# Performance work log

Hardware: AMD Instinct MI355X
Metric: run time of the kernel (lower is better)

The kernel has to match this reference:

```python
import jax, jax.numpy as jnp
import numpy as np

N = 100000   # nodes
E = 1600000  # edges
IN = 128     # input_dim
H = 64       # hidden_dim
C = 10       # num_classes
L = 4        # num_layers
G = 200      # graphs in batch
BN_EPS = 1e-5


def setup_inputs() -> dict:
    key = jax.random.key(0)
    ks = jax.random.split(key, 12)
    s = 0.05
    h = jax.random.normal(ks[0], (N, IN), jnp.float32)
    snorm_n = jax.random.uniform(ks[1], (N, 1), jnp.float32)
    src = jax.random.randint(ks[2], (E,), 0, N, jnp.int32)
    dst = jax.random.randint(ks[3], (E,), 0, N, jnp.int32)
    graph_ids = jnp.sort(jax.random.randint(ks[4], (N,), 0, G, jnp.int32))
    W_embed = jax.random.normal(ks[5], (IN, H), jnp.float32) * s
    b_embed = jnp.zeros((H,), jnp.float32)
    eps = jnp.zeros((L,), jnp.float32)               # learnable eps, init 0
    W1 = jax.random.normal(ks[6], (L, H, H), jnp.float32) * s
    b1 = jnp.zeros((L, H), jnp.float32)
    g1 = jnp.ones((L, H), jnp.float32)               # MLP-internal BN gamma
    be1 = jnp.zeros((L, H), jnp.float32)             # MLP-internal BN beta
    W2 = jax.random.normal(ks[7], (L, H, H), jnp.float32) * s
    b2 = jnp.zeros((L, H), jnp.float32)
    g2 = jnp.ones((L, H), jnp.float32)               # bn_node_h gamma
    be2 = jnp.zeros((L, H), jnp.float32)             # bn_node_h beta
    Wlin = jax.random.normal(ks[8], (L + 1, H, C), jnp.float32) * s
    blin = jnp.zeros((L + 1, C), jnp.float32)
    return dict(h=h, snorm_n=snorm_n, src=src, dst=dst, graph_ids=graph_ids,
                W_embed=W_embed, b_embed=b_embed, eps=eps,
                W1=W1, b1=b1, g1=g1, be1=be1, W2=W2, b2=b2, g2=g2, be2=be2,
                Wlin=Wlin, blin=blin)


def _batchnorm(x, gamma, beta):
    # training-mode BatchNorm1d over the node axis
    m = jnp.mean(x, axis=0)
    v = jnp.mean(jnp.square(x - m), axis=0)
    return gamma * (x - m) * jax.lax.rsqrt(v + BN_EPS) + beta


def reference(h, snorm_n, src, dst, graph_ids, W_embed, b_embed, eps,
              W1, b1, g1, be1, W2, b2, g2, be2, Wlin, blin):
    # node embedding
    h = h @ W_embed + b_embed                                   # [N, H]
    hidden_rep = [h]
    for i in range(L):
        h_in = h
        # copy_u + sum reduce: neigh[v] = sum_{(u->v)} h[u]
        neigh = jax.ops.segment_sum(h[src], dst, num_segments=N)  # [N, H]
        h = (1.0 + eps[i]) * h + neigh
        # apply_func: 2-layer MLP with internal BN+ReLU (standard GIN MLP)
        h = jax.nn.relu(_batchnorm(h @ W1[i] + b1[i], g1[i], be1[i]))
        h = h @ W2[i] + b2[i]
        h = h * snorm_n                                          # graph_norm
        h = _batchnorm(h, g2[i], be2[i])                         # bn_node_h
        h = jax.nn.relu(h)
        h = h_in + h                                             # residual
        # dropout p=0.0 -> identity
        hidden_rep.append(h)
    score = jnp.zeros((G, C), h.dtype)
    for i, hr in enumerate(hidden_rep):
        pooled = jax.ops.segment_sum(hr, graph_ids, num_segments=G)  # SumPooling
        score = score + pooled @ Wlin[i] + blin[i]
    return score
```

## Files before the change

### kernel.cpp

```cpp
#include <hip/hip_runtime.h>
#include <hip/hip_bf16.h>
#include <math.h>

#define NN 100000
#define NE 1600000
#define KIN 128
#define HD 64
#define NC 10
#define NL 4
#define NG 200
#define NBKT 196

typedef short s16x8 __attribute__((ext_vector_type(8)));
typedef float f32x4 __attribute__((ext_vector_type(4)));
using f4 = float4;

static __device__ __forceinline__ ushort f2bf(float x) {
  __hip_bfloat16 b = __float2bfloat16(x);
  return *reinterpret_cast<ushort*>(&b);
}
static __device__ __forceinline__ float bf2f(ushort u) {
  return __uint_as_float(((unsigned)u) << 16);
}
static __device__ __forceinline__ s16x8 zero8() {
  s16x8 v;
#pragma unroll
  for (int i = 0; i < 8; ++i) v[i] = 0;
  return v;
}

__global__ __launch_bounds__(256) void bucket_hist(const int* __restrict__ dst,
                                                   int* __restrict__ gbucket) {
  __shared__ int lh[NBKT];
  int tid = threadIdx.x;
  for (int i = tid; i < NBKT; i += 256) lh[i] = 0;
  __syncthreads();
  int base = blockIdx.x * 4096;
#pragma unroll 4
  for (int it = 0; it < 16; ++it) {
    int e = base + it * 256 + tid;
    if (e < NE) atomicAdd(&lh[dst[e] >> 9], 1);
  }
  __syncthreads();
  for (int i = tid; i < NBKT; i += 256)
    if (lh[i]) atomicAdd(&gbucket[i], lh[i]);
}

__global__ __launch_bounds__(256) void bucket_scan(const int* __restrict__ gbucket,
                                                   int* __restrict__ bbase,
                                                   int* __restrict__ bcur) {
  __shared__ int s[256];
  int tid = threadIdx.x;
  int v = (tid < NBKT) ? gbucket[tid] : 0;
  s[tid] = v;
  __syncthreads();
  for (int off = 1; off < 256; off <<= 1) {
    int t = (tid >= off) ? s[tid - off] : 0;
    __syncthreads();
    s[tid] += t;
    __syncthreads();
  }
  int excl = s[tid] - v;
  if (tid <= NBKT) bbase[tid] = excl;
  if (tid < NBKT) bcur[tid] = excl;
}

__global__ __launch_bounds__(256) void bucket_scatter(const int* __restrict__ src,
                                                      const int* __restrict__ dst,
                                                      int* __restrict__ bcur,
                                                      int2* __restrict__ pairs) {
  __shared__ int lh[NBKT];
  __shared__ int lbase[NBKT];
  int tid = threadIdx.x;
  for (int i = tid; i < NBKT; i += 256) lh[i] = 0;
  __syncthreads();
  int base = blockIdx.x * 4096;
  int dloc[16], sloc[16];
#pragma unroll
  for (int it = 0; it < 16; ++it) {
    int e = base + it * 256 + tid;
    bool ok = e < NE;
    dloc[it] = ok ? dst[e] : -1;
    sloc[it] = ok ? src[e] : 0;
    if (ok) atomicAdd(&lh[dloc[it] >> 9], 1);
  }
  __syncthreads();
  for (int i = tid; i < NBKT; i += 256) {
    int c = lh[i];
    lbase[i] = c ? atomicAdd(&bcur[i], c) : 0;
    lh[i] = 0;
  }
  __syncthreads();
#pragma unroll
  for (int it = 0; it < 16; ++it) {
    int d = dloc[it];
    if (d >= 0) {
      int b = d >> 9;
      int p = lbase[b] + atomicAdd(&lh[b], 1);
      pairs[p] = make_int2(d, sloc[it]);
    }
  }
}

__global__ __launch_bounds__(256) void csr_build(const int2* __restrict__ pairs,
                                                 const int* __restrict__ bbase,
                                                 int* __restrict__ row_ptr,
                                                 int* __restrict__ csr_src) {
  __shared__ int deg[512];
  __shared__ int psum[256];
  __shared__ int cur[512];
  int b = blockIdx.x;
  int tid = threadIdx.x;
  int beg = bbase[b], end = bbase[b + 1];
  int node0 = b << 9;
  deg[tid] = 0;
  deg[tid + 256] = 0;
  __syncthreads();
  for (int i = beg + tid; i < end; i += 256)
    atomicAdd(&deg[pairs[i].x - node0], 1);
  __syncthreads();
  int a0 = deg[2 * tid], a1 = deg[2 * tid + 1];
  psum[tid] = a0 + a1;
  __syncthreads();
  for (int off = 1; off < 256; off <<= 1) {
    int t = (tid >= off) ? psum[tid - off] : 0;
    __syncthreads();
    psum[tid] += t;
    __syncthreads();
  }
  int pe = psum[tid] - (a0 + a1);
  int e0 = pe, e1 = pe + a0;
  cur[2 * tid] = e0;
  cur[2 * tid + 1] = e1;
  int n0 = node0 + 2 * tid, n1 = node0 + 2 * tid + 1;
  if (n0 < NN) row_ptr[n0] = beg + e0;
  if (n1 < NN) row_ptr[n1] = beg + e1;
  __syncthreads();
  for (int i = beg + tid; i < end; i += 256) {
    int2 pr = pairs[i];
    int p = atomicAdd(&cur[pr.x - node0], 1);
    csr_src[beg + p] = pr.y;
  }
  if (b == 0 && tid == 0) row_ptr[NN] = NE;
}

__global__ __launch_bounds__(256) void pack_weights(
    const float* __restrict__ Wemb, const float* __restrict__ W1,
    const float* __restrict__ W2, ushort* __restrict__ Wpk) {
  int t = blockIdx.x;
  const float* src = (t < 2)   ? Wemb + t * 4096
                     : (t < 6) ? W1 + (t - 2) * 4096
                               : W2 + (t - 6) * 4096;
  for (int idx = threadIdx.x; idx < 4096; idx += 256) {
    int k = idx >> 6, n = idx & 63;
    int dsti = ((k >> 5) * 4 + (n >> 4)) * 512 +
               (((k >> 3) & 3) * 16 + (n & 15)) * 8 + (k & 7);
    Wpk[t * 4096 + dsti] = f2bf(src[idx]);
  }
}

__global__ __launch_bounds__(256) void pool_kernel(const ushort* __restrict__ hbf,
                                                   const int* __restrict__ gid,
                                                   float* __restrict__ pooledL) {
  int tid = threadIdx.x;
  int c = tid & 63;
  int rg = tid >> 6;
  int r0 = blockIdx.x * 128;
  int rend = r0 + 128 < NN ? r0 + 128 : NN;
  int rstart = r0 + rg;
  int cur = gid[rstart < NN ? rstart : NN - 1];
  float acc = 0.f;
  for (int r = rstart; r < rend; r += 4) {
    int g = gid[r];
    if (g != cur) {
      atomicAdd(&pooledL[cur * HD + c], acc);
      acc = 0.f;
      cur = g;
    }
    acc += bf2f(hbf[(size_t)r * HD + c]);
  }
  atomicAdd(&pooledL[cur * HD + c], acc);
}

__global__ __launch_bounds__(256) void gather_kernel(
    const ushort* __restrict__ hbf, const int* __restrict__ rp,
    const int* __restrict__ csrc, const float* __restrict__ eps_p,
    ushort* __restrict__ aggbf) {
  int node = blockIdx.x * 32 + (threadIdx.x >> 3);
  int lane = threadIdx.x & 7;
  if (node >= NN) return;
  int beg = rp[node], end = rp[node + 1];
  float epsv = 1.0f + eps_p[0];
  f4 sv = *reinterpret_cast<const f4*>(&hbf[(size_t)node * HD + lane * 8]);
  const ushort* su = reinterpret_cast<const ushort*>(&sv);
  float acc[8];
#pragma unroll
  for (int j = 0; j < 8; ++j) acc[j] = epsv * bf2f(su[j]);
  int e = beg;
  for (; e + 1 < end; e += 2) {
    int s0 = csrc[e], s1 = csrc[e + 1];
    f4 v0 = *reinterpret_cast<const f4*>(&hbf[(size_t)s0 * HD + lane * 8]);
    f4 v1 = *reinterpret_cast<const f4*>(&hbf[(size_t)s1 * HD + lane * 8]);
    const ushort* u0 = reinterpret_cast<const ushort*>(&v0);
    const ushort* u1 = reinterpret_cast<const ushort*>(&v1);
#pragma unroll
    for (int j = 0; j < 8; ++j) acc[j] += bf2f(u0[j]) + bf2f(u1[j]);
  }
  if (e < end) {
    int s0 = csrc[e];
    f4 v0 = *reinterpret_cast<const f4*>(&hbf[(size_t)s0 * HD + lane * 8]);
    const ushort* u0 = reinterpret_cast<const ushort*>(&v0);
#pragma unroll
    for (int j = 0; j < 8; ++j) acc[j] += bf2f(u0[j]);
  }
  alignas(16) ushort us[8];
#pragma unroll
  for (int j = 0; j < 8; ++j) us[j] = f2bf(acc[j]);
  *reinterpret_cast<s16x8*>(&aggbf[(size_t)node * HD + lane * 8]) =
      *reinterpret_cast<const s16x8*>(us);
}

template <int MODE>
__global__ __launch_bounds__(256, 4) void gemm_kernel(
    const void* Xin, const ushort* __restrict__ wt,
    const float* __restrict__ bias, const float* __restrict__ bn_in,
    const float* __restrict__ g1p, const float* __restrict__ be1p,
    const float* __restrict__ snorm, float* out, float* __restrict__ bn_out,
    ushort* __restrict__ hbf) {
  __shared__ ushort lds_a[128 * 64];
  __shared__ ushort lds_b[4096];
  __shared__ float lds_red[2][4][64];
  __shared__ float lds_bn[2][64];

  const int tid = threadIdx.x;
  const int row0 = blockIdx.x * 128;
  const int w = tid >> 6;
  const int l = tid & 63;
  const int lr = l >> 4, lc = l & 15;

  if (MODE == 2) {
    if (tid < 64) {
      float s = bn_in[tid], q = bn_in[64 + tid];
      float m = s * (1.0f / NN);
      float r = rsqrtf(q * (1.0f / NN) - m * m + 1e-5f);
      float scl = g1p[tid] * r;
      lds_bn[0][tid] = scl;
      lds_bn[1][tid] = be1p[tid] - m * scl;
    }
    __syncthreads();
  }

  f32x4 acc[2][4];
#pragma unroll
  for (int mi = 0; mi < 2; ++mi)
#pragma unroll
    for (int nf = 0; nf < 4; ++nf)
#pragma unroll
      for (int r = 0; r < 4; ++r) acc[mi][nf][r] = 0.f;

  const int KT = (MODE == 0) ? 2 : 1;
  for (int kt = 0; kt < KT; ++kt) {
    if (kt) __syncthreads();
#pragma unroll
    for (int i = 0; i < 2; ++i) {
      int ch = i * 256 + tid;
      *reinterpret_cast<s16x8*>(&lds_b[ch * 8]) =
          *reinterpret_cast<const s16x8*>(&wt[kt * 4096 + ch * 8]);
    }
#pragma unroll
    for (int i = 0; i < 4; ++i) {
      int f8i = i * 256 + tid;
      int row = f8i >> 3, c8 = f8i & 7;
      int grow = row0 + row;
      s16x8 val = zero8();
      if (grow < NN) {
        if (MODE == 1) {
          val = *reinterpret_cast<const s16x8*>(
              reinterpret_cast<const ushort*>(Xin) + (size_t)grow * HD + c8 * 8);
        } else {
          const float* p =
              (MODE == 0)
                  ? reinterpret_cast<const float*>(Xin) + (size_t)grow * KIN + kt * 64 + c8 * 8
                  : reinterpret_cast<const float*>(Xin) + (size_t)grow * HD + c8 * 8;
          f4 x0 = *reinterpret_cast<const f4*>(p);
          f4 x1 = *reinterpret_cast<const f4*>(p + 4);
          float xv[8] = {x0.x, x0.y, x0.z, x0.w, x1.x, x1.y, x1.z, x1.w};
          if (MODE == 2) {
#pragma unroll
            for (int j = 0; j < 8; ++j) {
              int c = c8 * 8 + j;
              float v = xv[j] * lds_bn[0][c] + lds_bn[1][c];
              xv[j] = v > 0.f ? v : 0.f;
            }
          }
          alignas(16) ushort us[8];
#pragma unroll
          for (int j = 0; j < 8; ++j) us[j] = f2bf(xv[j]);
          val = *reinterpret_cast<const s16x8*>(us);
        }
      }
      int slot = c8 ^ (row & 7);
      *reinterpret_cast<s16x8*>(&lds_a[row * 64 + slot * 8]) = val;
    }
    __syncthreads();

    s16x8 af[2][2];
#pragma unroll
    for (int mi = 0; mi < 2; ++mi)
#pragma unroll
      for (int kh = 0; kh < 2; ++kh) {
        int row = w * 32 + mi * 16 + lc;
        int slot = (kh * 4 + lr) ^ (row & 7);
        af[mi][kh] = *reinterpret_cast<const s16x8*>(&lds_a[row * 64 + slot * 8]);
      }
#pragma unroll
    for (int kh = 0; kh < 2; ++kh)
#pragma unroll
      for (int nf = 0; nf < 4; ++nf) {
        s16x8 bf = *reinterpret_cast<const s16x8*>(&lds_b[(kh * 4 + nf) * 512 + l * 8]);
#pragma unroll
        for (int mi = 0; mi < 2; ++mi)
          acc[mi][nf] = __builtin_amdgcn_mfma_f32_16x16x32_bf16(
              af[mi][kh], bf, acc[mi][nf], 0, 0, 0);
      }
  }

  float bias_l[4];
#pragma unroll
  for (int nf = 0; nf < 4; ++nf) bias_l[nf] = bias[nf * 16 + lc];

  float psum[4] = {0.f, 0.f, 0.f, 0.f}, psq[4] = {0.f, 0.f, 0.f, 0.f};
#pragma unroll
  for (int mi = 0; mi < 2; ++mi)
#pragma unroll
    for (int r = 0; r < 4; ++r) {
      int grow = row0 + w * 32 + mi * 16 + lr * 4 + r;
      if (grow < NN) {
        float sn = (MODE == 2) ? snorm[grow] : 1.0f;
#pragma unroll
        for (int nf = 0; nf < 4; ++nf) {
          float v = acc[mi][nf][r] + bias_l[nf];
          if (MODE == 2) v *= sn;
          if (MODE == 0) {
            hbf[(size_t)grow * HD + nf * 16 + lc] = f2bf(v);
          } else {
            out[(size_t)grow * HD + nf * 16 + lc] = v;
            psum[nf] += v;
            psq[nf] += v * v;
          }
        }
      }
    }
  if (MODE != 0) {
#pragma unroll
    for (int nf = 0; nf < 4; ++nf) {
      psum[nf] += __shfl_xor(psum[nf], 16);
      psq[nf] += __shfl_xor(psq[nf], 16);
      psum[nf] += __shfl_xor(psum[nf], 32);
      psq[nf] += __shfl_xor(psq[nf], 32);
    }
    if (l < 16) {
#pragma unroll
      for (int nf = 0; nf < 4; ++nf) {
        lds_red[0][w][nf * 16 + l] = psum[nf];
        lds_red[1][w][nf * 16 + l] = psq[nf];
      }
    }
    __syncthreads();
    if (tid < 64) {
      float s = 0.f, q = 0.f;
#pragma unroll
      for (int w2 = 0; w2 < 4; ++w2) {
        s += lds_red[0][w2][tid];
        q += lds_red[1][w2][tid];
      }
      atomicAdd(&bn_out[tid], s);
      atomicAdd(&bn_out[64 + tid], q);
    }
  }
}

__global__ __launch_bounds__(256) void final_pool_kernel(
    const float* __restrict__ t2, ushort* __restrict__ hbf,
    const float* __restrict__ g2p, const float* __restrict__ be2p,
    const float* __restrict__ stats2, const int* __restrict__ gid,
    float* __restrict__ pooledL) {
  int tid = threadIdx.x;
  int c = tid & 63;
  int rg = tid >> 6;
  float s = stats2[c], q = stats2[64 + c];
  float m = s * (1.0f / NN);
  float rr = rsqrtf(q * (1.0f / NN) - m * m + 1e-5f);
  float scl = g2p[c] * rr;
  float shv = be2p[c] - m * scl;
  int r0 = blockIdx.x * 128;
  int rend = r0 + 128 < NN ? r0 + 128 : NN;
  int rstart = r0 + rg;
  int cur = gid[rstart < NN ? rstart : NN - 1];
  float pacc = 0.f;
  for (int r = rstart; r < rend; r += 4) {
    int g = gid[r];
    if (g != cur) {
      atomicAdd(&pooledL[cur * HD + c], pacc);
      pacc = 0.f;
      cur = g;
    }
    float v = t2[(size_t)r * HD + c] * scl + shv;
    v = v > 0.f ? v : 0.f;
    float nv = bf2f(hbf[(size_t)r * HD + c]) + v;
    hbf[(size_t)r * HD + c] = f2bf(nv);
    pacc += nv;
  }
  atomicAdd(&pooledL[cur * HD + c], pacc);
}

__global__ __launch_bounds__(256) void score_kernel(
    const float* __restrict__ pooled, const float* __restrict__ Wlin,
    const float* __restrict__ blin, float* __restrict__ out) {
  int o = blockIdx.x * 256 + threadIdx.x;
  if (o >= NG * NC) return;
  int g = o / NC, c = o % NC;
  float s = 0.f;
  for (int i = 0; i <= NL; ++i) {
    s += blin[i * NC + c];
    const float* pg = &pooled[i * NG * HD + g * HD];
    const float* wl = &Wlin[i * HD * NC + c];
    float acc = 0.f;
#pragma unroll 8
    for (int k = 0; k < HD; ++k) acc += pg[k] * wl[k * NC];
    s += acc;
  }
  out[o] = s;
}

extern "C" void kernel_launch(void* const* d_in, const int* in_sizes, int n_in,
                              void* d_out, int out_size, void* d_ws,
                              size_t ws_size, hipStream_t stream) {
  const float* X = (const float*)d_in[0];
  const float* snorm = (const float*)d_in[1];
  const int* src = (const int*)d_in[2];
  const int* dst = (const int*)d_in[3];
  const int* gid = (const int*)d_in[4];
  const float* W_embed = (const float*)d_in[5];
  const float* b_embed = (const float*)d_in[6];
  const float* eps = (const float*)d_in[7];
  const float* W1 = (const float*)d_in[8];
  const float* b1 = (const float*)d_in[9];
  const float* g1 = (const float*)d_in[10];
  const float* be1 = (const float*)d_in[11];
  const float* W2 = (const float*)d_in[12];
  const float* b2 = (const float*)d_in[13];
  const float* g2 = (const float*)d_in[14];
  const float* be2 = (const float*)d_in[15];
  const float* Wlin = (const float*)d_in[16];
  const float* blin = (const float*)d_in[17];

  float* ws = (float*)d_ws;
  float* t1 = ws;
  float* pooled = t1 + (size_t)NN * HD;
  float* stats = pooled + 5 * NG * HD;
  int* ib = (int*)(stats + NL * 256);
  int* row_ptr = ib;
  int* gbucket = ib + 100004;
  int* bbase = ib + 100200;
  int* bcur = ib + 100400;
  int* csr_src = ib + 100600;
  ushort* h_bf = (ushort*)(ib + 100600 + NE);
  ushort* agg_bf = h_bf + (size_t)NN * HD;
  ushort* Wpk = agg_bf + (size_t)NN * HD;
  int2* pairs = (int2*)t1;

  const int GEMM_GRID = (NN + 127) / 128;
  const int EBLK = (NE + 4095) / 4096;
  const int POOL_GRID = (NN + 127) / 128;

  hipMemsetAsync(pooled, 0, (5 * NG * HD + NL * 256) * sizeof(float), stream);
  hipMemsetAsync(gbucket, 0, NBKT * sizeof(int), stream);

  pack_weights<<<10, 256, 0, stream>>>(W_embed, W1, W2, Wpk);

  bucket_hist<<<EBLK, 256, 0, stream>>>(dst, gbucket);
  bucket_scan<<<1, 256, 0, stream>>>(gbucket, bbase, bcur);
  bucket_scatter<<<EBLK, 256, 0, stream>>>(src, dst, bcur, pairs);
  csr_build<<<NBKT, 256, 0, stream>>>(pairs, bbase, row_ptr, csr_src);

  gemm_kernel<0><<<GEMM_GRID, 256, 0, stream>>>(
      X, Wpk, b_embed, nullptr, nullptr, nullptr, nullptr, nullptr, nullptr,
      h_bf);
  pool_kernel<<<POOL_GRID, 256, 0, stream>>>(h_bf, gid, pooled);

  for (int l = 0; l < NL; ++l) {
    float* st1 = stats + l * 256;
    float* st2 = stats + l * 256 + 128;
    gather_kernel<<<(NN + 31) / 32, 256, 0, stream>>>(h_bf, row_ptr, csr_src,
                                                      eps + l, agg_bf);
    gemm_kernel<1><<<GEMM_GRID, 256, 0, stream>>>(
        agg_bf, Wpk + (2 + l) * 4096, b1 + l * 64, nullptr, nullptr, nullptr,
        nullptr, t1, st1, nullptr);
    gemm_kernel<2><<<GEMM_GRID, 256, 0, stream>>>(
        t1, Wpk + (6 + l) * 4096, b2 + l * 64, st1, g1 + l * 64, be1 + l * 64,
        snorm, t1, st2, nullptr);
    final_pool_kernel<<<POOL_GRID, 256, 0, stream>>>(
        t1, h_bf, g2 + l * 64, be2 + l * 64, st2, gid,
        pooled + (l + 1) * NG * HD);
  }

  score_kernel<<<(NG * NC + 255) / 256, 256, 0, stream>>>(pooled, Wlin, blin,
                                                          (float*)d_out);
}
```

Baseline: 625.2 us.

## Fuse neighbor gather into first MLP GEMM and store intermediates in bf16

```diff
diff --git a/kernel.cpp b/kernel.cpp
--- a/kernel.cpp
+++ b/kernel.cpp
@@ -182,51 +182,14 @@
   atomicAdd(&pooledL[cur * HD + c], acc);
 }
 
-__global__ __launch_bounds__(256) void gather_kernel(
-    const ushort* __restrict__ hbf, const int* __restrict__ rp,
-    const int* __restrict__ csrc, const float* __restrict__ eps_p,
-    ushort* __restrict__ aggbf) {
-  int node = blockIdx.x * 32 + (threadIdx.x >> 3);
-  int lane = threadIdx.x & 7;
-  if (node >= NN) return;
-  int beg = rp[node], end = rp[node + 1];
-  float epsv = 1.0f + eps_p[0];
-  f4 sv = *reinterpret_cast<const f4*>(&hbf[(size_t)node * HD + lane * 8]);
-  const ushort* su = reinterpret_cast<const ushort*>(&sv);
-  float acc[8];
-#pragma unroll
-  for (int j = 0; j < 8; ++j) acc[j] = epsv * bf2f(su[j]);
-  int e = beg;
-  for (; e + 1 < end; e += 2) {
-    int s0 = csrc[e], s1 = csrc[e + 1];
-    f4 v0 = *reinterpret_cast<const f4*>(&hbf[(size_t)s0 * HD + lane * 8]);
-    f4 v1 = *reinterpret_cast<const f4*>(&hbf[(size_t)s1 * HD + lane * 8]);
-    const ushort* u0 = reinterpret_cast<const ushort*>(&v0);
-    const ushort* u1 = reinterpret_cast<const ushort*>(&v1);
-#pragma unroll
-    for (int j = 0; j < 8; ++j) acc[j] += bf2f(u0[j]) + bf2f(u1[j]);
-  }
-  if (e < end) {
-    int s0 = csrc[e];
-    f4 v0 = *reinterpret_cast<const f4*>(&hbf[(size_t)s0 * HD + lane * 8]);
-    const ushort* u0 = reinterpret_cast<const ushort*>(&v0);
-#pragma unroll
-    for (int j = 0; j < 8; ++j) acc[j] += bf2f(u0[j]);
-  }
-  alignas(16) ushort us[8];
-#pragma unroll
-  for (int j = 0; j < 8; ++j) us[j] = f2bf(acc[j]);
-  *reinterpret_cast<s16x8*>(&aggbf[(size_t)node * HD + lane * 8]) =
-      *reinterpret_cast<const s16x8*>(us);
-}
-
 template <int MODE>
 __global__ __launch_bounds__(256, 4) void gemm_kernel(
     const void* Xin, const ushort* __restrict__ wt,
     const float* __restrict__ bias, const float* __restrict__ bn_in,
     const float* __restrict__ g1p, const float* __restrict__ be1p,
-    const float* __restrict__ snorm, float* out, float* __restrict__ bn_out,
-    ushort* __restrict__ hbf) {
+    const float* __restrict__ snorm, const int* __restrict__ rp,
+    const int* __restrict__ csrc, const float* __restrict__ eps_p,
+    ushort* __restrict__ outbf, float* __restrict__ bn_out) {
   __shared__ ushort lds_a[128 * 64];
   __shared__ ushort lds_b[4096];
   __shared__ float lds_red[2][4][64];
@@ -267,40 +230,76 @@
       *reinterpret_cast<s16x8*>(&lds_b[ch * 8]) =
           *reinterpret_cast<const s16x8*>(&wt[kt * 4096 + ch * 8]);
     }
-#pragma unroll
-    for (int i = 0; i < 4; ++i) {
-      int f8i = i * 256 + tid;
-      int row = f8i >> 3, c8 = f8i & 7;
-      int grow = row0 + row;
-      s16x8 val = zero8();
-      if (grow < NN) {
-        if (MODE == 1) {
-          val = *reinterpret_cast<const s16x8*>(
-              reinterpret_cast<const ushort*>(Xin) + (size_t)grow * HD + c8 * 8);
-        } else {
-          const float* p =
-              (MODE == 0)
-                  ? reinterpret_cast<const float*>(Xin) + (size_t)grow * KIN + kt * 64 + c8 * 8
-                  : reinterpret_cast<const float*>(Xin) + (size_t)grow * HD + c8 * 8;
-          f4 x0 = *reinterpret_cast<const f4*>(p);
-          f4 x1 = *reinterpret_cast<const f4*>(p + 4);
-          float xv[8] = {x0.x, x0.y, x0.z, x0.w, x1.x, x1.y, x1.z, x1.w};
-          if (MODE == 2) {
+    if (MODE == 1) {
+      const ushort* hbf = reinterpret_cast<const ushort*>(Xin);
+      float epsv = 1.0f + eps_p[0];
+      int lane = tid & 7;
+#pragma unroll
+      for (int g = 0; g < 4; ++g) {
+        int row = g * 32 + (tid >> 3);
+        int grow = row0 + row;
+        s16x8 val = zero8();
+        if (grow < NN) {
+          int beg = rp[grow], end = rp[grow + 1];
+          f4 sv = *reinterpret_cast<const f4*>(&hbf[(size_t)grow * HD + lane * 8]);
+          const ushort* su = reinterpret_cast<const ushort*>(&sv);
+          float a8[8];
+#pragma unroll
+          for (int j = 0; j < 8; ++j) a8[j] = epsv * bf2f(su[j]);
+          int e = beg;
+          for (; e + 1 < end; e += 2) {
+            int s0 = csrc[e], s1 = csrc[e + 1];
+            f4 v0 = *reinterpret_cast<const f4*>(&hbf[(size_t)s0 * HD + lane * 8]);
+            f4 v1 = *reinterpret_cast<const f4*>(&hbf[(size_t)s1 * HD + lane * 8]);
+            const ushort* u0 = reinterpret_cast<const ushort*>(&v0);
+            const ushort* u1 = reinterpret_cast<const ushort*>(&v1);
+#pragma unroll
+            for (int j = 0; j < 8; ++j) a8[j] += bf2f(u0[j]) + bf2f(u1[j]);
+          }
+          if (e < end) {
+            int s0 = csrc[e];
+            f4 v0 = *reinterpret_cast<const f4*>(&hbf[(size_t)s0 * HD + lane * 8]);
+            const ushort* u0 = reinterpret_cast<const ushort*>(&v0);
+#pragma unroll
+            for (int j = 0; j < 8; ++j) a8[j] += bf2f(u0[j]);
+          }
+#pragma unroll
+          for (int j = 0; j < 8; ++j) val[j] = (short)f2bf(a8[j]);
+        }
+        int slot = lane ^ (row & 7);
+        *reinterpret_cast<s16x8*>(&lds_a[row * 64 + slot * 8]) = val;
+      }
+    } else {
+#pragma unroll
+      for (int i = 0; i < 4; ++i) {
+        int f8i = i * 256 + tid;
+        int row = f8i >> 3, c8 = f8i & 7;
+        int grow = row0 + row;
+        s16x8 val = zero8();
+        if (grow < NN) {
+          if (MODE == 0) {
+            const float* p =
+                reinterpret_cast<const float*>(Xin) + (size_t)grow * KIN + kt * 64 + c8 * 8;
+            f4 x0 = *reinterpret_cast<const f4*>(p);
+            f4 x1 = *reinterpret_cast<const f4*>(p + 4);
+            float xv[8] = {x0.x, x0.y, x0.z, x0.w, x1.x, x1.y, x1.z, x1.w};
+#pragma unroll
+            for (int j = 0; j < 8; ++j) val[j] = (short)f2bf(xv[j]);
+          } else {
+            s16x8 raw = *reinterpret_cast<const s16x8*>(
+                reinterpret_cast<const ushort*>(Xin) + (size_t)grow * HD + c8 * 8);
 #pragma unroll
             for (int j = 0; j < 8; ++j) {
               int c = c8 * 8 + j;
-              float v = xv[j] * lds_bn[0][c] + lds_bn[1][c];
-              xv[j] = v > 0.f ? v : 0.f;
+              float v = bf2f((ushort)raw[j]) * lds_bn[0][c] + lds_bn[1][c];
+              v = v > 0.f ? v : 0.f;
+              val[j] = (short)f2bf(v);
             }
           }
-          alignas(16) ushort us[8];
-#pragma unroll
-          for (int j = 0; j < 8; ++j) us[j] = f2bf(xv[j]);
-          val = *reinterpret_cast<const s16x8*>(us);
         }
-      }
-      int slot = c8 ^ (row & 7);
-      *reinterpret_cast<s16x8*>(&lds_a[row * 64 + slot * 8]) = val;
+        int slot = c8 ^ (row & 7);
+        *reinterpret_cast<s16x8*>(&lds_a[row * 64 + slot * 8]) = val;
+      }
     }
     __syncthreads();
 
@@ -341,10 +340,8 @@
         for (int nf = 0; nf < 4; ++nf) {
           float v = acc[mi][nf][r] + bias_l[nf];
           if (MODE == 2) v *= sn;
-          if (MODE == 0) {
-            hbf[(size_t)grow * HD + nf * 16 + lc] = f2bf(v);
-          } else {
-            out[(size_t)grow * HD + nf * 16 + lc] = v;
+          outbf[(size_t)grow * HD + nf * 16 + lc] = f2bf(v);
+          if (MODE != 0) {
             psum[nf] += v;
             psq[nf] += v * v;
           }
@@ -381,7 +378,7 @@
 }
 
 __global__ __launch_bounds__(256) void final_pool_kernel(
-    const float* __restrict__ t2, ushort* __restrict__ hbf,
+    const ushort* __restrict__ t2bf, ushort* __restrict__ hbf,
     const float* __restrict__ g2p, const float* __restrict__ be2p,
     const float* __restrict__ stats2, const int* __restrict__ gid,
     float* __restrict__ pooledL) {
@@ -405,7 +402,7 @@
       pacc = 0.f;
       cur = g;
     }
-    float v = t2[(size_t)r * HD + c] * scl + shv;
+    float v = bf2f(t2bf[(size_t)r * HD + c]) * scl + shv;
     v = v > 0.f ? v : 0.f;
     float nv = bf2f(hbf[(size_t)r * HD + c]) + v;
     hbf[(size_t)r * HD + c] = f2bf(nv);
@@ -456,8 +453,8 @@
   const float* blin = (const float*)d_in[17];
 
   float* ws = (float*)d_ws;
-  float* t1 = ws;
-  float* pooled = t1 + (size_t)NN * HD;
+  float* scratch = ws;
+  float* pooled = scratch + (size_t)NN * HD;
   float* stats = pooled + 5 * NG * HD;
   int* ib = (int*)(stats + NL * 256);
   int* row_ptr = ib;
@@ -466,9 +463,9 @@
   int* bcur = ib + 100400;
   int* csr_src = ib + 100600;
   ushort* h_bf = (ushort*)(ib + 100600 + NE);
-  ushort* agg_bf = h_bf + (size_t)NN * HD;
-  ushort* Wpk = agg_bf + (size_t)NN * HD;
-  int2* pairs = (int2*)t1;
+  ushort* t1bf = h_bf + (size_t)NN * HD;
+  ushort* Wpk = t1bf + (size_t)NN * HD;
+  int2* pairs = (int2*)scratch;
 
   const int GEMM_GRID = (NN + 127) / 128;
   const int EBLK = (NE + 4095) / 4096;
@@ -486,22 +483,20 @@
 
   gemm_kernel<0><<<GEMM_GRID, 256, 0, stream>>>(
       X, Wpk, b_embed, nullptr, nullptr, nullptr, nullptr, nullptr, nullptr,
-      h_bf);
+      nullptr, h_bf, nullptr);
   pool_kernel<<<POOL_GRID, 256, 0, stream>>>(h_bf, gid, pooled);
 
   for (int l = 0; l < NL; ++l) {
     float* st1 = stats + l * 256;
     float* st2 = stats + l * 256 + 128;
-    gather_kernel<<<(NN + 31) / 32, 256, 0, stream>>>(h_bf, row_ptr, csr_src,
-                                                      eps + l, agg_bf);
     gemm_kernel<1><<<GEMM_GRID, 256, 0, stream>>>(
-        agg_bf, Wpk + (2 + l) * 4096, b1 + l * 64, nullptr, nullptr, nullptr,
-        nullptr, t1, st1, nullptr);
+        h_bf, Wpk + (2 + l) * 4096, b1 + l * 64, nullptr, nullptr, nullptr,
+        nullptr, row_ptr, csr_src, eps + l, t1bf, st1);
     gemm_kernel<2><<<GEMM_GRID, 256, 0, stream>>>(
-        t1, Wpk + (6 + l) * 4096, b2 + l * 64, st1, g1 + l * 64, be1 + l * 64,
-        snorm, t1, st2, nullptr);
+        t1bf, Wpk + (6 + l) * 4096, b2 + l * 64, st1, g1 + l * 64,
+        be1 + l * 64, snorm, nullptr, nullptr, nullptr, t1bf, st2);
     final_pool_kernel<<<POOL_GRID, 256, 0, stream>>>(
-        t1, h_bf, g2 + l * 64, be2 + l * 64, st2, gid,
+        t1bf, h_bf, g2 + l * 64, be2 + l * 64, st2, gid,
         pooled + (l + 1) * NG * HD);
   }
 
```

New measurement: 577.6 us. 7.6% less time.
